# Optimization experiments

Hardware: AMD Instinct MI355X
Metric: run time of the kernel (lower is better)

The kernel has to match this reference:

```python
import jax, jax.numpy as jnp
import numpy as np

U10_IDX, V10_IDX = 0, 1
WIND_THRESH = 0.5


def _gru(x, h, Wih, Whh, bih, bhh):
    # standard torch GRUCell math
    gi = x @ Wih.T + bih
    gh = h @ Whh.T + bhh
    ir, iz, inn = jnp.split(gi, 3, axis=-1)
    hr, hz, hnn = jnp.split(gh, 3, axis=-1)
    r = jax.nn.sigmoid(ir + hr)
    z = jax.nn.sigmoid(iz + hz)
    n = jnp.tanh(inn + r * hnn)
    return (1.0 - z) * n + z * h


def setup_inputs() -> dict:
    B, N, H, F, Th, Tf = 256, 184, 128, 8, 24, 24
    key = jax.random.key(0)
    ks = jax.random.split(key, 24)
    s = 0.1
    f32 = jnp.float32
    feature = jax.random.normal(ks[0], (B, Th + Tf, N, F), f32)
    pm25_hist = jax.random.uniform(ks[1], (B, Th, N, 1), dtype=f32)
    adj_mat = (jax.random.uniform(ks[2], (N, N)) < 0.1).astype(f32)
    angles = jax.random.uniform(ks[3], (N, N), f32, 0.0, 2.0 * np.pi)
    C = F + 1  # ChebConv in-channels = in_dim + out_dim
    return dict(
        feature=feature, pm25_hist=pm25_hist, adj_mat=adj_mat, angles=angles,
        W_ih_hist=s * jax.random.normal(ks[4], (3 * H, 2), f32),
        W_hh_hist=s * jax.random.normal(ks[5], (3 * H, H), f32),
        b_ih_hist=s * jax.random.normal(ks[6], (3 * H,), f32),
        b_hh_hist=s * jax.random.normal(ks[7], (3 * H,), f32),
        fc_hist_w=s * jax.random.normal(ks[8], (1, H), f32),
        fc_hist_b=s * jax.random.normal(ks[9], (1,), f32),
        cheb_w0=s * jax.random.normal(ks[10], (C, 1), f32),
        cheb_w1=s * jax.random.normal(ks[11], (C, 1), f32),
        cheb_b=s * jax.random.normal(ks[12], (1,), f32),
        W_ih=s * jax.random.normal(ks[13], (3 * H, C + 1), f32),
        W_hh=s * jax.random.normal(ks[14], (3 * H, H), f32),
        b_ih=s * jax.random.normal(ks[15], (3 * H,), f32),
        b_hh=s * jax.random.normal(ks[16], (3 * H,), f32),
        fc_out_w=s * jax.random.normal(ks[17], (1, H), f32),
        fc_out_b=s * jax.random.normal(ks[18], (1,), f32),
    )


def reference(feature, pm25_hist, adj_mat, angles,
              W_ih_hist, W_hh_hist, b_ih_hist, b_hh_hist,
              fc_hist_w, fc_hist_b,
              cheb_w0, cheb_w1, cheb_b,
              W_ih, W_hh, b_ih, b_hh,
              fc_out_w, fc_out_b):
    B, T, N, F = feature.shape
    H = W_hh.shape[1]
    Th = pm25_hist.shape[1]
    comp1 = jnp.cos(angles)                                # [N,N]
    comp2 = jnp.cos(angles - jnp.float32(np.pi / 2.0))     # [N,N]
    adj_b = adj_mat > 0

    # ---- history GRU over pm25_hist ----
    def hist_step(carry, p):
        hn, xn = carry
        x = jnp.concatenate([xn, p], axis=-1).reshape(B * N, 2)
        hn = _gru(x, hn, W_ih_hist, W_hh_hist, b_ih_hist, b_hh_hist)
        xn = hn.reshape(B, N, H) @ fc_hist_w.T + fc_hist_b
        return (hn, xn), None

    h0 = jnp.zeros((B * N, H), feature.dtype)
    x0 = jnp.zeros((B, N, 1), feature.dtype)
    (hn, xn), _ = jax.lax.scan(hist_step, (h0, x0), jnp.swapaxes(pm25_hist, 0, 1))

    # ---- forecast: dynamic wind-gated graph + ChebConv(K=2) + GRU ----
    def fore_step(carry, f):
        hn, xn = carry
        x = jnp.concatenate([xn, f], axis=-1)              # [B,N,F+1]
        u = f[..., U10_IDX]                                # [B,N]
        v = f[..., V10_IDX]
        wind = u[:, :, None] * comp1[None] + v[:, :, None] * comp2[None]
        # edge i->j iff adj and wind projection >= threshold
        M = jnp.logical_and(wind >= WIND_THRESH, adj_b[None]).astype(x.dtype)
        deg = M.sum(-1)                                    # source degree [B,N]
        has = deg > 0
        dinv = jnp.where(has, 1.0 / jnp.sqrt(jnp.where(has, deg, 1.0)), 0.0)
        # ChebConv scaled Laplacian (lambda_max=2, sym norm):
        # L_hat x [j] = -dinv_j * sum_i dinv_i * M[i,j] * x[i] + (0 if deg_j>0 else -1) * x[j]
        y = jnp.einsum('bij,bic->bjc', M * dinv[:, :, None], x)
        y = -dinv[:, :, None] * y + jnp.where(has, 0.0, -1.0)[:, :, None] * x
        g = jax.nn.sigmoid(x @ cheb_w0 + y @ cheb_w1 + cheb_b)  # [B,N,1]
        x2 = jnp.concatenate([x, g], axis=-1).reshape(B * N, F + 2)
        hn = _gru(x2, hn, W_ih, W_hh, b_ih, b_hh)
        xn = hn.reshape(B, N, H) @ fc_out_w.T + fc_out_b
        return (hn, xn), xn

    fore_feat = jnp.swapaxes(feature[:, Th:], 0, 1)        # [Tf,B,N,F]
    (_, _), preds = jax.lax.scan(fore_step, (hn, xn), fore_feat)
    return jnp.swapaxes(preds, 0, 1)                       # [B,Tf,N,1]
```

## Files before the change

kernel.cpp:

```cpp
#include <hip/hip_runtime.h>
#include <hip/hip_bf16.h>
#include <math.h>

#define BB 256
#define NN 184
#define HH 128
#define FF 8
#define TH 24
#define TF 24
#define KA 160
#define NG2 640
#define RPAD 192
#define STRH 136
#define NT 1024
#define NW3 552
#define LOG2E 1.44269504088896f

#define REC_F 8832
#define OFF_DINV 4416
#define OFF_G 5152
#define OFF_AXF 5888

typedef __attribute__((ext_vector_type(8))) short bf16x8;
typedef __attribute__((ext_vector_type(4))) short bf16x4;
typedef __attribute__((ext_vector_type(4))) float f32x4;
typedef __attribute__((ext_vector_type(2))) unsigned u32x2;

#if __has_builtin(__builtin_amdgcn_mfma_f32_16x16x16bf16_1k)
#define XK16 1
#else
#define XK16 0
#endif

#if __has_builtin(__builtin_amdgcn_exp2f)
#define EXP2(x) __builtin_amdgcn_exp2f(x)
#else
#define EXP2(x) exp2f(x)
#endif

__device__ __forceinline__ unsigned short f2bf(float f) {
    unsigned u = __float_as_uint(f);
    u += 0x7fffu + ((u >> 16) & 1u);
    return (unsigned short)(u >> 16);
}
__device__ __forceinline__ unsigned pkbf(float a, float b) {
    __hip_bfloat162 h = __float22bfloat162_rn(make_float2(a, b));
    return *reinterpret_cast<unsigned*>(&h);
}
__device__ __forceinline__ void gload16(const void* src, void* dst) {
    __builtin_amdgcn_global_load_lds(
        (const __attribute__((address_space(1))) unsigned int*)src,
        (__attribute__((address_space(3))) unsigned int*)dst, 16, 0, 0);
}

__global__ void prep_weights(const float* __restrict__ WhhH, const float* __restrict__ WihH,
                             const float* __restrict__ WhhF, const float* __restrict__ WihF,
                             const float* __restrict__ bihH, const float* __restrict__ bhhH,
                             const float* __restrict__ bihF, const float* __restrict__ bhhF,
                             const float* __restrict__ fchw, const float* __restrict__ fchb,
                             unsigned short* __restrict__ WaH, unsigned short* __restrict__ WaF) {
    int idx = blockIdx.x * 256 + threadIdx.x;
    if (idx >= NG2 * KA) return;
    int jp = idx / KA, k = idx % KA;
    int j = jp & 127, part = jp >> 7;
    float vh = 0.f, vf = 0.f;
    if (part <= 1) {
        int row = part * 128 + j;
        if (k < 128) {
            vh = WhhH[row * 128 + k] + WihH[row * 2 + 0] * fchw[k];
            vf = WhhF[row * 128 + k];
        } else {
            int s = k - 128;
            if (s == 0)  vh = WihH[row * 2 + 1];
            if (s < 8)   vf = WihF[row * 10 + (s + 1)];
            if (s == 8)  { vh = WihH[row * 2 + 0]; vf = WihF[row * 10 + 0]; }
            if (s == 9)  vf = WihF[row * 10 + 9];
            if (s == 11) {
                vh = bihH[row] + bhhH[row] + WihH[row * 2 + 0] * fchb[0];
                vf = bihF[row] + bhhF[row];
            }
        }
    } else if (part == 2) {
        if (k < 128) { vh = WhhH[(256 + j) * 128 + k]; vf = WhhF[(256 + j) * 128 + k]; }
        else if (k == 139) { vh = bhhH[256 + j]; vf = bhhF[256 + j]; }
    } else if (part == 3) {
        if (k >= 128) {
            int s = k - 128;
            if (s == 0)  vh = WihH[(256 + j) * 2 + 1];
            if (s < 8)   vf = WihF[(256 + j) * 10 + (s + 1)];
            if (s == 8)  { vh = WihH[(256 + j) * 2 + 0]; vf = WihF[(256 + j) * 10 + 0]; }
            if (s == 9)  vf = WihF[(256 + j) * 10 + 9];
            if (s == 11) {
                vh = bihH[256 + j] + WihH[(256 + j) * 2 + 0] * fchb[0];
                vf = bihF[256 + j];
            }
        }
    } else {
        if (k < 128) vh = WihH[(256 + j) * 2 + 0] * fchw[k];
    }
    float sc = (part <= 1) ? LOG2E : 2.0f * LOG2E;
    WaH[idx] = f2bf(vh * sc);
    WaF[idx] = f2bf(vf * sc);
}

__global__ void prep_edges(const float* __restrict__ angles, const float* __restrict__ adj,
                           float4* __restrict__ edges, int* __restrict__ cnt) {
    int idx = blockIdx.x * 256 + threadIdx.x;
    if (idx < NN * NN && adj[idx] > 0.f) {
        float a = angles[idx];
        int pos = atomicAdd(cnt, 1);
        float4 r;
        r.x = cosf(a);
        r.y = cosf(a - 1.57079632679489662f);
        r.z = __int_as_float(idx / NN);
        r.w = __int_as_float(idx % NN);
        edges[pos] = r;
    }
}

__global__ void prep_hist(const float* __restrict__ pm25, unsigned short* __restrict__ phist) {
    int idx = blockIdx.x * 256 + threadIdx.x;
    if (idx < BB * TH * NN) phist[idx] = f2bf(pm25[idx]);
}

__global__ __launch_bounds__(256) void prep_graph(
    const float* __restrict__ feature,
    const float4* __restrict__ edges, const int* __restrict__ ecnt,
    const float* __restrict__ cw0, const float* __restrict__ cw1,
    const float* __restrict__ cbb, char* __restrict__ xrec)
{
    const int bt = blockIdx.x;
    const int b = bt / TF, tf = bt % TF;
    const int tt = TH + tf;
    const int tid = threadIdx.x;

    char* rec = xrec + ((long)b * TF + tf) * REC_F;

    __shared__ float f8[NN * FF];
    __shared__ unsigned long long mT[NN][3];
    __shared__ int dg[NN];
    __shared__ float di[NN];
    __shared__ float sI[NN];
    __shared__ float red[NW3];

    const float4* fb4 = (const float4*)(feature + ((long)b * (TH + TF) + tt) * (NN * FF));
    for (int i = tid; i < (NN * FF) / 4; i += 256) ((float4*)f8)[i] = fb4[i];
    for (int i = tid; i < NN * 3; i += 256) ((unsigned long long*)mT)[i] = 0ull;
    for (int i = tid; i < NN; i += 256) dg[i] = 0;
    __syncthreads();
    const int nE = *ecnt;
    for (int e = tid; e < nE; e += 256) {
        float4 r = edges[e];
        int ii = __float_as_int(r.z), jj = __float_as_int(r.w);
        if (f8[ii * FF] * r.x + f8[ii * FF + 1] * r.y >= 0.5f) {
            atomicAdd(&dg[ii], 1);
            atomicOr(&mT[jj][ii >> 6], 1ull << (ii & 63));
        }
    }
    __syncthreads();
    if (tid < NN) {
        float d = (dg[tid] > 0) ? rsqrtf((float)dg[tid]) : 0.f;
        di[tid] = d;
        float s = 0.f;
        #pragma unroll
        for (int c = 0; c < 8; ++c) s = fmaf(f8[tid * FF + c], cw1[c + 1], s);
        sI[tid] = d * s;
    }
    __syncthreads();
    unsigned long long* mr = (unsigned long long*)rec;
    for (int i = tid; i < NW3; i += 256) mr[i] = ((const unsigned long long*)mT)[i];
    for (int task = tid; task < NW3; task += 256) {
        int j = task / 3, wd = task - j * 3;
        unsigned long long m = mT[j][wd];
        float acc = 0.f;
        while (m) {
            int bp = __ffsll(m) - 1; m &= m - 1;
            acc += sI[wd * 64 + bp];
        }
        red[task] = acc;
    }
    __syncthreads();
    if (tid < NN) {
        int j = tid;
        float dj = di[j];
        float hzj = (dj > 0.f) ? 0.f : -1.f;
        float S0 = 0.f, S1 = 0.f;
        #pragma unroll
        for (int c = 0; c < 8; ++c) {
            float xv = f8[j * FF + c];
            S0 = fmaf(xv, cw0[c + 1], S0);
            S1 = fmaf(xv, cw1[c + 1], S1);
        }
        float G = cbb[0] + S0 + hzj * S1
                - dj * (red[j * 3 + 0] + red[j * 3 + 1] + red[j * 3 + 2]);
        ((float*)(rec + OFF_DINV))[j] = dj;
        ((float*)(rec + OFF_G))[j] = G;
        unsigned short* ax = (unsigned short*)(rec + OFF_AXF) + j * 8;
        #pragma unroll
        for (int c = 0; c < 8; ++c) ax[c] = f2bf(f8[j * FF + c]);
    }
}

__global__ __launch_bounds__(NT, 4) void fused_dgc(
    const unsigned short* __restrict__ WaH,
    const unsigned short* __restrict__ WaF,
    const float* __restrict__ fchw, const float* __restrict__ fchb,
    const float* __restrict__ fcow, const float* __restrict__ fcob,
    const float* __restrict__ cw0, const float* __restrict__ cw1,
    const char* __restrict__ xrec, const unsigned short* __restrict__ phist,
    float* __restrict__ pred)
{
    __shared__ unsigned short Ah[2][RPAD * STRH];
    __shared__ unsigned short AxR[RPAD * 8];
    __shared__ __align__(16) char stg[2][8960];
    __shared__ float xnraw[2][RPAD];
    __shared__ float fcls_f[132];
    __shared__ unsigned short zero16[8];
    __shared__ __align__(16) unsigned short phist_s[TH * NN + 16];

    const int tid = threadIdx.x;
    const int bb = blockIdx.x;
    const int w = tid >> 6, lane = tid & 63, q = lane >> 4, lq = lane & 15;
    const int cg = w & 7, rh = w >> 3;

    for (int i = tid; i < RPAD * STRH; i += NT) Ah[0][i] = 0;
    for (int i = tid; i < RPAD * 8; i += NT)
        AxR[i] = ((i & 7) == 3) ? (unsigned short)0x3F80 : (unsigned short)0;
    if (tid < 8) zero16[tid] = 0;
    if (tid < RPAD) { xnraw[0][tid] = 0.f; xnraw[1][tid] = 0.f; }

    bf16x8 wregH[4][4];
#if XK16
    bf16x4 wregX[4];
#else
    bf16x8 wregX[4];
#endif
    auto load_w = [&](const unsigned short* Wa, const float* fcw, const float* fcb, bool h4) {
        const int jcol = cg * 16 + lq;
        #pragma unroll
        for (int g = 0; g < 3; ++g)
            #pragma unroll
            for (int kc = 0; kc < 4; ++kc)
                wregH[g][kc] = *(const bf16x8*)(Wa + (long)(g * 128 + jcol) * KA + kc * 32 + q * 8);
        if (h4)
            #pragma unroll
            for (int kc = 0; kc < 4; ++kc)
                wregH[3][kc] = *(const bf16x8*)(Wa + (long)(4 * 128 + jcol) * KA + kc * 32 + q * 8);
        #pragma unroll
        for (int g = 0; g < 4; ++g)
#if XK16
            wregX[g] = *(const bf16x4*)(Wa + (long)(g * 128 + jcol) * KA + 128 + q * 4);
#else
            wregX[g] = *(const bf16x8*)(Wa + (long)(g * 128 + jcol) * KA + 128 + q * 8);
#endif
        if (tid < 132) fcls_f[tid] = (tid < 128) ? fcw[tid] : ((tid == 128) ? fcb[0] : 0.f);
    };
    load_w(WaH, fchw, fchb, true);

    if (tid < NW3)
        gload16((const char*)phist + (long)bb * (TH * NN * 2) + tid * 16,
                (char*)phist_s + (tid & ~63) * 16);

    const float w00 = cw0[0], w10 = cw1[0];
    const float fcbH = fchb[0], fcbO = fcob[0];
    const f32x4 zf = {0.f, 0.f, 0.f, 0.f};

    int p = 0;
    __syncthreads();

    for (int t = 0; t < TH + TF; ++t) {
        const bool hist = (t < TH);
        const bool dofc = (t >= TH - 1);
        const unsigned short* AxFS = (const unsigned short*)(stg[p] + OFF_AXF);

        if (!hist) {
            const unsigned long long* maskS = (const unsigned long long*)stg[p];
            const float* dinS = (const float*)(stg[p] + OFF_DINV);
            const float* GS = (const float*)(stg[p] + OFF_G);
            const float* xr = xnraw[(t - 1) & 1];
            const float fcbP = (t == TH) ? fcbH : fcbO;
            const int jg = tid >> 2, wd = tid & 3;
            if (jg < NN) {
                float acc = 0.f, accd = 0.f;
                if (wd < 3) {
                    unsigned long long m = maskS[jg * 3 + wd];
                    while (m) {
                        int bp = __ffsll(m) - 1; m &= m - 1;
                        int i = wd * 64 + bp;
                        float d = dinS[i];
                        acc = fmaf(d, xr[i], acc);
                        accd += d;
                    }
                }
                acc  += __shfl_xor(acc, 1);  acc  += __shfl_xor(acc, 2);
                accd += __shfl_xor(accd, 1); accd += __shfl_xor(accd, 2);
                if (wd == 0) {
                    float dj = dinS[jg];
                    float xnj = xr[jg] + fcbP;
                    float hzj = (dj > 0.f) ? 0.f : -1.f;
                    float sum = fmaf(fcbP, accd, acc);
                    float y0 = -dj * sum + hzj * xnj;
                    float pre = GS[jg] + xnj * w00 + y0 * w10;
                    float g = __builtin_amdgcn_rcpf(1.0f + EXP2(-LOG2E * pre));
                    AxR[jg * 8 + 1] = f2bf(g);
                    AxR[jg * 8 + 0] = f2bf(xnj);
                    if (t > TH) pred[((long)bb * TF + (t - 1 - TH)) * NN + jg] = xnj;
                }
            } else {
                int i = tid - 736;
                if (i < RPAD) xnraw[t & 1][i] = 0.f;
            }
            __syncthreads();
        }

        const int t2 = t + 1;
        if (t2 >= TH && t2 < TH + TF && tid < NW3)
            gload16(xrec + ((long)bb * TF + (t2 - TH)) * REC_F + tid * 16,
                    (char*)stg[p ^ 1] + (tid & ~63) * 16);

        f32x4 fw = *(const f32x4*)&fcls_f[cg * 16 + q * 4];
        const unsigned short corr0 = (t == 0) ? f2bf(-fcbH) : (unsigned short)0;
        #pragma unroll
        for (int rl = 0; rl < 6; ++rl) {
            const int row = rh * 96 + rl * 16 + lq;
            const int ro = row * STRH;
            f32x4 a0, a1, a2, a3;
            {
                bf16x8 bh = *(const bf16x8*)(&Ah[p][ro + q * 8]);
                a0 = __builtin_amdgcn_mfma_f32_16x16x32_bf16(wregH[0][0], bh, zf, 0, 0, 0);
                a1 = __builtin_amdgcn_mfma_f32_16x16x32_bf16(wregH[1][0], bh, zf, 0, 0, 0);
                a2 = __builtin_amdgcn_mfma_f32_16x16x32_bf16(wregH[2][0], bh, zf, 0, 0, 0);
                a3 = hist ? __builtin_amdgcn_mfma_f32_16x16x32_bf16(wregH[3][0], bh, zf, 0, 0, 0)
                          : zf;
            }
            #pragma unroll
            for (int kc = 1; kc < 4; ++kc) {
                bf16x8 bh = *(const bf16x8*)(&Ah[p][ro + kc * 32 + q * 8]);
                a0 = __builtin_amdgcn_mfma_f32_16x16x32_bf16(wregH[0][kc], bh, a0, 0, 0, 0);
                a1 = __builtin_amdgcn_mfma_f32_16x16x32_bf16(wregH[1][kc], bh, a1, 0, 0, 0);
                a2 = __builtin_amdgcn_mfma_f32_16x16x32_bf16(wregH[2][kc], bh, a2, 0, 0, 0);
                if (hist)
                    a3 = __builtin_amdgcn_mfma_f32_16x16x32_bf16(wregH[3][kc], bh, a3, 0, 0, 0);
            }
#if XK16
            bf16x4 bx;
            if (hist) {
                unsigned short pb = phist_s[t * NN + row];
                bf16x4 z = {0,0,0,0};
                bx = z;
                if (q == 0) bx[0] = (short)pb;
                if (q == 2) { bx[0] = (short)corr0; bx[3] = (short)0x3F80; }
            } else {
                const unsigned short* bxp = (q < 2) ? (AxFS + row * 8 + q * 4)
                                          : (q == 2) ? (AxR + row * 8) : zero16;
                bx = *(const bf16x4*)bxp;
            }
            a0 = __builtin_amdgcn_mfma_f32_16x16x16bf16_1k(wregX[0], bx, a0, 0, 0, 0);
            a1 = __builtin_amdgcn_mfma_f32_16x16x16bf16_1k(wregX[1], bx, a1, 0, 0, 0);
            a2 = __builtin_amdgcn_mfma_f32_16x16x16bf16_1k(wregX[2], bx, a2, 0, 0, 0);
            a3 = __builtin_amdgcn_mfma_f32_16x16x16bf16_1k(wregX[3], bx, a3, 0, 0, 0);
#else
            bf16x8 bx;
            if (hist) {
                unsigned short pb = phist_s[t * NN + row];
                bf16x8 z = {0,0,0,0,0,0,0,0};
                bx = z;
                if (q == 0) bx[0] = (short)pb;
                if (q == 1) { bx[0] = (short)corr0; bx[3] = (short)0x3F80; }
            } else {
                const unsigned short* bxp = (q == 0) ? (AxFS + row * 8)
                                          : (q == 1) ? (AxR + row * 8) : zero16;
                bx = *(const bf16x8*)bxp;
            }
            a0 = __builtin_amdgcn_mfma_f32_16x16x32_bf16(wregX[0], bx, a0, 0, 0, 0);
            a1 = __builtin_amdgcn_mfma_f32_16x16x32_bf16(wregX[1], bx, a1, 0, 0, 0);
            a2 = __builtin_amdgcn_mfma_f32_16x16x32_bf16(wregX[2], bx, a2, 0, 0, 0);
            a3 = __builtin_amdgcn_mfma_f32_16x16x32_bf16(wregX[3], bx, a3, 0, 0, 0);
#endif

            u32x2 hold = *(const u32x2*)&Ah[p][ro + cg * 16 + q * 4];

            float hn[4];
            #pragma unroll
            for (int rg = 0; rg < 4; ++rg) {
                unsigned hu = hold[rg >> 1];
                float ho = ((rg & 1) == 0) ? __uint_as_float(hu << 16)
                                           : __uint_as_float(hu & 0xffff0000u);
                float rr = __builtin_amdgcn_rcpf(1.0f + EXP2(-a0[rg]));
                float zz = __builtin_amdgcn_rcpf(1.0f + EXP2(-a1[rg]));
                float wv = fmaf(rr, a2[rg], a3[rg]);
                float s2 = __builtin_amdgcn_rcpf(1.0f + EXP2(-wv));
                float tv = fmaf(2.0f, s2, -1.0f);
                hn[rg] = fmaf(zz, ho - tv, tv);
            }
            u32x2 pk;
            pk[0] = pkbf(hn[0], hn[1]);
            pk[1] = pkbf(hn[2], hn[3]);
            *(u32x2*)&Ah[p ^ 1][ro + cg * 16 + q * 4] = pk;
            if (dofc) {
                float pf = hn[0] * fw.x + hn[1] * fw.y + hn[2] * fw.z + hn[3] * fw.w;
                pf += __shfl_xor(pf, 16);
                pf += __shfl_xor(pf, 32);
                if (q == 0) atomicAdd(&xnraw[t & 1][row], pf);
            }
        }
        __syncthreads();

        if (t == TH - 1)
            load_w(WaF, fcow, fcob, false);
        p ^= 1;
    }

    if (tid < NN)
        pred[((long)bb * TF + (TF - 1)) * NN + tid] =
            xnraw[(TH + TF - 1) & 1][tid] + fcbO;
}

extern "C" void kernel_launch(void* const* d_in, const int* in_sizes, int n_in,
                              void* d_out, int out_size, void* d_ws, size_t ws_size,
                              hipStream_t stream) {
    const float* feature = (const float*)d_in[0];
    const float* pm25    = (const float*)d_in[1];
    const float* adj     = (const float*)d_in[2];
    const float* angles  = (const float*)d_in[3];
    const float* W_ih_h  = (const float*)d_in[4];
    const float* W_hh_h  = (const float*)d_in[5];
    const float* b_ih_h  = (const float*)d_in[6];
    const float* b_hh_h  = (const float*)d_in[7];
    const float* fch_w   = (const float*)d_in[8];
    const float* fch_b   = (const float*)d_in[9];
    const float* cw0     = (const float*)d_in[10];
    const float* cw1     = (const float*)d_in[11];
    const float* cbb     = (const float*)d_in[12];
    const float* W_ih    = (const float*)d_in[13];
    const float* W_hh    = (const float*)d_in[14];
    const float* b_ih    = (const float*)d_in[15];
    const float* b_hh    = (const float*)d_in[16];
    const float* fco_w   = (const float*)d_in[17];
    const float* fco_b   = (const float*)d_in[18];
    float* pred = (float*)d_out;

    char* ws = (char*)d_ws;
    size_t off = 0;
    unsigned short* WaH   = (unsigned short*)(ws + off); off += (size_t)NG2 * KA * 2;
    unsigned short* WaF   = (unsigned short*)(ws + off); off += (size_t)NG2 * KA * 2;
    float4*         edges = (float4*)(ws + off);         off += (size_t)NN * NN * 16;
    int*            cnt   = (int*)(ws + off);            off += 16;
    unsigned short* phist = (unsigned short*)(ws + off); off += (size_t)BB * TH * NN * 2;
    char*           xrec  = (char*)(ws + off);
    off += (size_t)BB * TF * REC_F;

    hipMemsetAsync(cnt, 0, 16, stream);
    prep_weights<<<(NG2 * KA + 255) / 256, 256, 0, stream>>>(
        W_hh_h, W_ih_h, W_hh, W_ih, b_ih_h, b_hh_h, b_ih, b_hh, fch_w, fch_b,
        WaH, WaF);
    prep_edges<<<(NN * NN + 255) / 256, 256, 0, stream>>>(angles, adj, edges, cnt);
    prep_hist<<<(BB * TH * NN + 255) / 256, 256, 0, stream>>>(pm25, phist);
    prep_graph<<<BB * TF, 256, 0, stream>>>(
        feature, edges, cnt, cw0, cw1, cbb, xrec);

    fused_dgc<<<BB, NT, 0, stream>>>(
        WaH, WaF, fch_w, fch_b, fco_w, fco_b, cw0, cw1, xrec, phist, pred);
}
```

Measured before the change: 573.1 us.

## Fuse graph-record and pm25 history prep into the recurrent kernel's history steps

Removes the separate prep_hist and prep_graph kernels. During each history timestep, the main recurrent kernel now builds the wind-gated adjacency mask, degrees and Chebyshev gate record for the matching forecast step, and writes it to the workspace for later use. It also converts pm25 history to bf16 directly into shared memory. This drops two launches and a global round trip of the converted history, and hides the graph work behind the history recurrence. In exchange it adds extra shared memory and extra barriers inside the history loop, which may lower occupancy or lengthen each history step. It also depends on the same block's global writes being visible when the forecast steps read them back.

```diff
diff --git a/kernel.cpp b/kernel.cpp
--- a/kernel.cpp
+++ b/kernel.cpp
@@ -118,96 +118,16 @@
     }
 }
 
-__global__ void prep_hist(const float* __restrict__ pm25, unsigned short* __restrict__ phist) {
-    int idx = blockIdx.x * 256 + threadIdx.x;
-    if (idx < BB * TH * NN) phist[idx] = f2bf(pm25[idx]);
-}
-
-__global__ __launch_bounds__(256) void prep_graph(
-    const float* __restrict__ feature,
-    const float4* __restrict__ edges, const int* __restrict__ ecnt,
-    const float* __restrict__ cw0, const float* __restrict__ cw1,
-    const float* __restrict__ cbb, char* __restrict__ xrec)
-{
-    const int bt = blockIdx.x;
-    const int b = bt / TF, tf = bt % TF;
-    const int tt = TH + tf;
-    const int tid = threadIdx.x;
-
-    char* rec = xrec + ((long)b * TF + tf) * REC_F;
-
-    __shared__ float f8[NN * FF];
-    __shared__ unsigned long long mT[NN][3];
-    __shared__ int dg[NN];
-    __shared__ float di[NN];
-    __shared__ float sI[NN];
-    __shared__ float red[NW3];
-
-    const float4* fb4 = (const float4*)(feature + ((long)b * (TH + TF) + tt) * (NN * FF));
-    for (int i = tid; i < (NN * FF) / 4; i += 256) ((float4*)f8)[i] = fb4[i];
-    for (int i = tid; i < NN * 3; i += 256) ((unsigned long long*)mT)[i] = 0ull;
-    for (int i = tid; i < NN; i += 256) dg[i] = 0;
-    __syncthreads();
-    const int nE = *ecnt;
-    for (int e = tid; e < nE; e += 256) {
-        float4 r = edges[e];
-        int ii = __float_as_int(r.z), jj = __float_as_int(r.w);
-        if (f8[ii * FF] * r.x + f8[ii * FF + 1] * r.y >= 0.5f) {
-            atomicAdd(&dg[ii], 1);
-            atomicOr(&mT[jj][ii >> 6], 1ull << (ii & 63));
-        }
-    }
-    __syncthreads();
-    if (tid < NN) {
-        float d = (dg[tid] > 0) ? rsqrtf((float)dg[tid]) : 0.f;
-        di[tid] = d;
-        float s = 0.f;
-        #pragma unroll
-        for (int c = 0; c < 8; ++c) s = fmaf(f8[tid * FF + c], cw1[c + 1], s);
-        sI[tid] = d * s;
-    }
-    __syncthreads();
-    unsigned long long* mr = (unsigned long long*)rec;
-    for (int i = tid; i < NW3; i += 256) mr[i] = ((const unsigned long long*)mT)[i];
-    for (int task = tid; task < NW3; task += 256) {
-        int j = task / 3, wd = task - j * 3;
-        unsigned long long m = mT[j][wd];
-        float acc = 0.f;
-        while (m) {
-            int bp = __ffsll(m) - 1; m &= m - 1;
-            acc += sI[wd * 64 + bp];
-        }
-        red[task] = acc;
-    }
-    __syncthreads();
-    if (tid < NN) {
-        int j = tid;
-        float dj = di[j];
-        float hzj = (dj > 0.f) ? 0.f : -1.f;
-        float S0 = 0.f, S1 = 0.f;
-        #pragma unroll
-        for (int c = 0; c < 8; ++c) {
-            float xv = f8[j * FF + c];
-            S0 = fmaf(xv, cw0[c + 1], S0);
-            S1 = fmaf(xv, cw1[c + 1], S1);
-        }
-        float G = cbb[0] + S0 + hzj * S1
-                - dj * (red[j * 3 + 0] + red[j * 3 + 1] + red[j * 3 + 2]);
-        ((float*)(rec + OFF_DINV))[j] = dj;
-        ((float*)(rec + OFF_G))[j] = G;
-        unsigned short* ax = (unsigned short*)(rec + OFF_AXF) + j * 8;
-        #pragma unroll
-        for (int c = 0; c < 8; ++c) ax[c] = f2bf(f8[j * FF + c]);
-    }
-}
-
 __global__ __launch_bounds__(NT, 4) void fused_dgc(
     const unsigned short* __restrict__ WaH,
     const unsigned short* __restrict__ WaF,
     const float* __restrict__ fchw, const float* __restrict__ fchb,
     const float* __restrict__ fcow, const float* __restrict__ fcob,
     const float* __restrict__ cw0, const float* __restrict__ cw1,
-    const char* __restrict__ xrec, const unsigned short* __restrict__ phist,
+    const float* __restrict__ cbb,
+    const float* __restrict__ feature, const float* __restrict__ pm25,
+    const float4* __restrict__ edges, const int* __restrict__ ecnt,
+    char* __restrict__ xrec,
     float* __restrict__ pred)
 {
     __shared__ unsigned short Ah[2][RPAD * STRH];
@@ -217,6 +137,11 @@
     __shared__ float fcls_f[132];
     __shared__ unsigned short zero16[8];
     __shared__ __align__(16) unsigned short phist_s[TH * NN + 16];
+    __shared__ float f8[NN * FF];
+    __shared__ unsigned long long mT[NN * 3];
+    __shared__ int dg[NN];
+    __shared__ float2 dsI[NN];
+    __shared__ float cwS[17];
 
     const int tid = threadIdx.x;
     const int bb = blockIdx.x;
@@ -228,6 +153,19 @@
         AxR[i] = ((i & 7) == 3) ? (unsigned short)0x3F80 : (unsigned short)0;
     if (tid < 8) zero16[tid] = 0;
     if (tid < RPAD) { xnraw[0][tid] = 0.f; xnraw[1][tid] = 0.f; }
+    if (tid < 17)
+        cwS[tid] = (tid < 8) ? cw1[tid + 1] : ((tid < 16) ? cw0[tid - 7] : cbb[0]);
+
+    {
+        const float4* psrc = (const float4*)(pm25 + (long)bb * TH * NN);
+        for (int i = tid; i < (TH * NN) / 4; i += NT) {
+            float4 v = psrc[i];
+            u32x2 pk2;
+            pk2[0] = pkbf(v.x, v.y);
+            pk2[1] = pkbf(v.z, v.w);
+            *(u32x2*)&phist_s[i * 4] = pk2;
+        }
+    }
 
     bf16x8 wregH[4][4];
 #if XK16
@@ -257,10 +195,7 @@
     };
     load_w(WaH, fchw, fchb, true);
 
-    if (tid < NW3)
-        gload16((const char*)phist + (long)bb * (TH * NN * 2) + tid * 16,
-                (char*)phist_s + (tid & ~63) * 16);
-
+    const int nE = *ecnt;
     const float w00 = cw0[0], w10 = cw1[0];
     const float fcbH = fchb[0], fcbO = fcob[0];
     const f32x4 zf = {0.f, 0.f, 0.f, 0.f};
@@ -273,7 +208,67 @@
         const bool dofc = (t >= TH - 1);
         const unsigned short* AxFS = (const unsigned short*)(stg[p] + OFF_AXF);
 
-        if (!hist) {
+        if (hist) {
+            char* rec = xrec + ((long)bb * TF + t) * REC_F;
+            const float4* fsrc = (const float4*)(feature + ((long)bb * (TH + TF) + TH + t) * (NN * FF));
+            for (int i = tid; i < (NN * FF) / 4; i += NT) ((float4*)f8)[i] = fsrc[i];
+            for (int i = tid; i < NN * 3; i += NT) mT[i] = 0ull;
+            if (tid < NN) dg[tid] = 0;
+            __syncthreads();
+            for (int e = tid; e < nE; e += NT) {
+                float4 r = edges[e];
+                int ii = __float_as_int(r.z), jj = __float_as_int(r.w);
+                if (f8[ii * FF] * r.x + f8[ii * FF + 1] * r.y >= 0.5f) {
+                    atomicAdd(&dg[ii], 1);
+                    atomicOr(&mT[jj * 3 + (ii >> 6)], 1ull << (ii & 63));
+                }
+            }
+            __syncthreads();
+            if (tid < NN) {
+                float d = (dg[tid] > 0) ? rsqrtf((float)dg[tid]) : 0.f;
+                float s = 0.f;
+                #pragma unroll
+                for (int c = 0; c < 8; ++c) s = fmaf(f8[tid * FF + c], cwS[c], s);
+                dsI[tid] = make_float2(d, d * s);
+            }
+            __syncthreads();
+            {
+                const int jg = tid >> 2, wd = tid & 3;
+                if (jg < NN) {
+                    float acc = 0.f;
+                    if (wd < 3) {
+                        unsigned long long m = mT[jg * 3 + wd];
+                        ((unsigned long long*)rec)[jg * 3 + wd] = m;
+                        while (m) {
+                            int bp = __ffsll(m) - 1; m &= m - 1;
+                            acc += dsI[wd * 64 + bp].y;
+                        }
+                    }
+                    acc += __shfl_xor(acc, 1);
+                    acc += __shfl_xor(acc, 2);
+                    if (wd == 0) {
+                        float dj = dsI[jg].x;
+                        float hzj = (dj > 0.f) ? 0.f : -1.f;
+                        float S0 = 0.f, S1 = 0.f;
+                        #pragma unroll
+                        for (int c = 0; c < 8; ++c) {
+                            float xv = f8[jg * FF + c];
+                            S1 = fmaf(xv, cwS[c], S1);
+                            S0 = fmaf(xv, cwS[8 + c], S0);
+                        }
+                        float G = cwS[16] + S0 + hzj * S1 - dj * acc;
+                        ((float*)(rec + OFF_DINV))[jg] = dj;
+                        ((float*)(rec + OFF_G))[jg] = G;
+                        uint4 ax4;
+                        ax4.x = pkbf(f8[jg * FF + 0], f8[jg * FF + 1]);
+                        ax4.y = pkbf(f8[jg * FF + 2], f8[jg * FF + 3]);
+                        ax4.z = pkbf(f8[jg * FF + 4], f8[jg * FF + 5]);
+                        ax4.w = pkbf(f8[jg * FF + 6], f8[jg * FF + 7]);
+                        *(uint4*)(rec + OFF_AXF + jg * 16) = ax4;
+                    }
+                }
+            }
+        } else {
             const unsigned long long* maskS = (const unsigned long long*)stg[p];
             const float* dinS = (const float*)(stg[p] + OFF_DINV);
             const float* GS = (const float*)(stg[p] + OFF_G);
@@ -446,7 +441,6 @@
     unsigned short* WaF   = (unsigned short*)(ws + off); off += (size_t)NG2 * KA * 2;
     float4*         edges = (float4*)(ws + off);         off += (size_t)NN * NN * 16;
     int*            cnt   = (int*)(ws + off);            off += 16;
-    unsigned short* phist = (unsigned short*)(ws + off); off += (size_t)BB * TH * NN * 2;
     char*           xrec  = (char*)(ws + off);
     off += (size_t)BB * TF * REC_F;
 
@@ -455,10 +449,8 @@
         W_hh_h, W_ih_h, W_hh, W_ih, b_ih_h, b_hh_h, b_ih, b_hh, fch_w, fch_b,
         WaH, WaF);
     prep_edges<<<(NN * NN + 255) / 256, 256, 0, stream>>>(angles, adj, edges, cnt);
-    prep_hist<<<(BB * TH * NN + 255) / 256, 256, 0, stream>>>(pm25, phist);
-    prep_graph<<<BB * TF, 256, 0, stream>>>(
-        feature, edges, cnt, cw0, cw1, cbb, xrec);
 
     fused_dgc<<<BB, NT, 0, stream>>>(
-        WaH, WaF, fch_w, fch_b, fco_w, fco_b, cw0, cw1, xrec, phist, pred);
-}
+        WaH, WaF, fch_w, fch_b, fco_w, fco_b, cw0, cw1, cbb,
+        feature, pm25, edges, cnt, xrec, pred);
+}
```

Measured after the change: 633.1 us. 1.1x slower.
